# Performance work log

Measured on AMD Instinct MI355X. Metric: run time of the kernel, lower is better.

The kernel has to match this reference:

```python
import jax, jax.numpy as jnp
import numpy as np

BATCH = 8192
IN_DIM = 2048
OUT_DIM = 2048
DEPTH = 5


def setup_inputs() -> dict:
    key = jax.random.key(0)
    k1, k2, k3, k4 = jax.random.split(key, 4)
    x = jax.random.normal(k1, (BATCH, IN_DIM), dtype=jnp.float32)
    hyperdimensional_weights = jax.random.normal(k2, (DEPTH, IN_DIM, OUT_DIM), dtype=jnp.float32)
    classical_weights = jax.random.normal(k3, (IN_DIM, OUT_DIM), dtype=jnp.float32)
    classical_biases = jax.random.normal(k4, (OUT_DIM,), dtype=jnp.float32)
    return {
        "x": x,
        "hyperdimensional_weights": hyperdimensional_weights,
        "classical_weights": classical_weights,
        "classical_biases": classical_biases,
    }


def _hyperdimensional_probs(hd_w):
    # angle = W[d, j, 0], phase = W[d, j, 1] for output index j (j < input_dims)
    depth, in_dim, _ = hd_w.shape
    angles = hd_w[:, :OUT_DIM, 0]   # [depth, out]
    phases = hd_w[:, :OUT_DIM, 1]   # [depth, out]
    # Initial uniform state 1/sqrt(n), replicated per output unit j.
    s0 = jnp.full((OUT_DIM, in_dim), 1.0 / np.sqrt(in_dim), dtype=jnp.complex64)

    def step(s, ang_ph):
        ang, ph = ang_ph                      # each [out]
        c = jnp.cos(ang)[:, None]
        sn = jnp.sin(ang)[:, None]
        # Circulant rotation: new[k] = cos*s[k] - sin*s[k+1] + sin*s[k-1] (cyclic)
        s = c * s - sn * jnp.roll(s, -1, axis=1) + sn * jnp.roll(s, 1, axis=1)
        # Global phase gate: diag(e^{i*phase})
        s = s * jnp.exp(1j * ph)[:, None]
        return s, None

    s, _ = jax.lax.scan(step, s0, (angles, phases))
    # probability = |state[0]|^2
    return jnp.abs(s[:, 0]) ** 2              # [out], real float32


def reference(x, hyperdimensional_weights, classical_weights, classical_biases):
    classical = x @ classical_weights + classical_biases            # [B, out]
    hd = _hyperdimensional_probs(hyperdimensional_weights)          # [out] (batch-independent)
    return jnp.tanh(classical + hd[None, :])
```

## Files before the change

kernel.cpp:

```cpp
#include <hip/hip_runtime.h>

#define BATCH 8192
#define DIM   2048
#define DEPTH 5


#define BUFSZ  65536
#define ABYTES 32768

typedef short bf16x8_t __attribute__((ext_vector_type(8)));
typedef float f32x4_t  __attribute__((ext_vector_type(4)));

__device__ __forceinline__ unsigned short f2bf(float f) {
  unsigned u = __float_as_uint(f);
  u += 0x7fffu + ((u >> 16) & 1u);
  return (unsigned short)(u >> 16);
}
__device__ __forceinline__ float bf2f(unsigned short h) {
  return __uint_as_float(((unsigned)h) << 16);
}

__global__ void prep_fused_kernel(const float* __restrict__ x,
                                  const float* __restrict__ hdw,
                                  const float* __restrict__ W,
                                  const float* __restrict__ bias,
                                  float* __restrict__ bias2,
                                  unsigned short* __restrict__ xhi,
                                  unsigned short* __restrict__ xlo,
                                  unsigned short* __restrict__ whi,
                                  unsigned short* __restrict__ wlo) {
  __shared__ float tile[32][33];
  const int b = blockIdx.x;
  const int tid = threadIdx.x;

  if (b < 8192) {
    size_t g = (size_t)b * 256 + tid;
    const float4* xp = (const float4*)(x + g * 8);
    float4 v0 = xp[0], v1 = xp[1];
    float v[8] = {v0.x, v0.y, v0.z, v0.w, v1.x, v1.y, v1.z, v1.w};
    bf16x8_t h, lo;
#pragma unroll
    for (int j = 0; j < 8; ++j) {
      unsigned short hj = f2bf(v[j]);
      h[j] = (short)hj;
      lo[j] = (short)f2bf(v[j] - bf2f(hj));
    }
    ((bf16x8_t*)xhi)[g] = h;
    ((bf16x8_t*)xlo)[g] = lo;
  } else if (b < 12288) {
    const int t = b - 8192;
    const int k0 = (t >> 6) * 32;
    const int n0 = (t & 63) * 32;
    const int tx = tid & 31;
    const int ty = tid >> 5;
#pragma unroll
    for (int r = 0; r < 32; r += 8)
      tile[ty + r][tx] = W[(size_t)(k0 + ty + r) * DIM + n0 + tx];
    __syncthreads();
    const int n = tid >> 3;
    const int kq = (tid & 7) * 4;
    ushort4 hv, lv;
    float vv0 = tile[kq + 0][n], vv1 = tile[kq + 1][n];
    float vv2 = tile[kq + 2][n], vv3 = tile[kq + 3][n];
    hv.x = f2bf(vv0); lv.x = f2bf(vv0 - bf2f(hv.x));
    hv.y = f2bf(vv1); lv.y = f2bf(vv1 - bf2f(hv.y));
    hv.z = f2bf(vv2); lv.z = f2bf(vv2 - bf2f(hv.z));
    hv.w = f2bf(vv3); lv.w = f2bf(vv3 - bf2f(hv.w));
    const size_t o = (size_t)(n0 + n) * DIM + k0 + kq;
    *(ushort4*)(whi + o) = hv;
    *(ushort4*)(wlo + o) = lv;
  } else {
    int j = (b - 12288) * 256 + tid;
    float p = 1.0f;
#pragma unroll
    for (int d = 0; d < DEPTH; ++d)
      p *= cosf(hdw[(size_t)d * DIM * DIM + (size_t)j * DIM]);
    bias2[j] = bias[j] + p * p * (1.0f / 2048.0f);
  }
}

#define GLDS(SRC, OFF)                                                         \
  __builtin_amdgcn_global_load_lds(                                            \
      (const __attribute__((address_space(1))) unsigned int*)(SRC),            \
      (__attribute__((address_space(3))) unsigned int*)(smem + (OFF)), 16, 0, 0)

#define MFMA16(A, B, C) __builtin_amdgcn_mfma_f32_16x16x32_bf16((A), (B), (C), 0, 0, 0)

#define STAGE(KO, SO)                                                          \
  do {                                                                         \
    GLDS(sAh + (KO),             (SO) + 0              + wdst);                \
    GLDS(sAh + 128 * DIM + (KO), (SO) + 8192           + wdst);                \
    GLDS(sAl + (KO),             (SO) + 16384          + wdst);                \
    GLDS(sAl + 128 * DIM + (KO), (SO) + 24576          + wdst);                \
    GLDS(sBh + (KO),             (SO) + ABYTES + 0     + wdst);                \
    GLDS(sBh + 128 * DIM + (KO), (SO) + ABYTES + 8192  + wdst);                \
    GLDS(sBl + (KO),             (SO) + ABYTES + 16384 + wdst);                \
    GLDS(sBl + 128 * DIM + (KO), (SO) + ABYTES + 24576 + wdst);                \
  } while (0)

__global__ __launch_bounds__(512, 2) void gemm_pipe_kernel(
    const unsigned short* __restrict__ Ah, const unsigned short* __restrict__ Al,
    const unsigned short* __restrict__ Bh, const unsigned short* __restrict__ Bl,
    const float* __restrict__ bias2, float* __restrict__ out) {
  __shared__ float4 smem4[2 * BUFSZ / 16];
  char* smem = (char*)smem4;

  const int tid  = threadIdx.x;
  const int lane = tid & 63;
  const int wave = tid >> 6;
  const int wm   = wave >> 1;
  const int wn   = wave & 1;
  const int l15  = lane & 15;
  const int kl   = lane >> 4;
  const int bm = blockIdx.x;
  const int bn = blockIdx.y;

  const int rsub = wave * 16 + (lane >> 2);
  const int kg   = ((lane & 3) ^ ((lane >> 3) & 3)) * 8;
  const unsigned short* sAh = Ah + ((size_t)(bm * 256 + rsub)) * DIM + kg;
  const unsigned short* sAl = Al + ((size_t)(bm * 256 + rsub)) * DIM + kg;
  const unsigned short* sBh = Bh + ((size_t)(bn * 256 + rsub)) * DIM + kg;
  const unsigned short* sBl = Bl + ((size_t)(bn * 256 + rsub)) * DIM + kg;
  const unsigned wdst = wave * 1024;

  const int foff = l15 * 64 + ((kl * 16) ^ (((l15 >> 1) & 3) << 4));

  const f32x4_t vzero = {0.f, 0.f, 0.f, 0.f};
  f32x4_t acc[4][8];
#pragma unroll
  for (int i = 0; i < 4; ++i)
#pragma unroll
    for (int j = 0; j < 8; ++j) acc[i][j] = vzero;

  STAGE(0, 0);
  asm volatile("s_waitcnt vmcnt(0)" ::: "memory");
  asm volatile("s_barrier" ::: "memory");

#pragma unroll 1
  for (int t = 0; t < 64; ++t) {
    const unsigned bo = (unsigned)(t & 1) * BUFSZ;
    const unsigned so = bo ^ BUFSZ;

    if (t < 63) {
      const int ko = (t + 1) * 32;
      STAGE(ko, so);
    }

    const char* pA = smem + bo + wm * 4096 + foff;
    bf16x8_t ah[4], al[4];
#pragma unroll
    for (int mt = 0; mt < 4; ++mt) {
      ah[mt] = *(const bf16x8_t*)(pA + mt * 1024);
      al[mt] = *(const bf16x8_t*)(pA + 16384 + mt * 1024);
    }

    const char* pB = smem + bo + ABYTES + wn * 8192 + foff;

    {
      bf16x8_t bh[4], bl[4];
#pragma unroll
      for (int nt = 0; nt < 4; ++nt) {
        bh[nt] = *(const bf16x8_t*)(pB + nt * 1024);
        bl[nt] = *(const bf16x8_t*)(pB + 16384 + nt * 1024);
      }
      __builtin_amdgcn_s_setprio(1);
#pragma unroll
      for (int mt = 0; mt < 4; ++mt)
#pragma unroll
        for (int nt = 0; nt < 4; ++nt) {
          acc[mt][nt] = MFMA16(ah[mt], bh[nt], acc[mt][nt]);
          acc[mt][nt] = MFMA16(ah[mt], bl[nt], acc[mt][nt]);
          acc[mt][nt] = MFMA16(al[mt], bh[nt], acc[mt][nt]);
        }
      __builtin_amdgcn_s_setprio(0);
    }

    {
      bf16x8_t bh[4], bl[4];
#pragma unroll
      for (int nt = 0; nt < 4; ++nt) {
        bh[nt] = *(const bf16x8_t*)(pB + 4096 + nt * 1024);
        bl[nt] = *(const bf16x8_t*)(pB + 16384 + 4096 + nt * 1024);
      }
      __builtin_amdgcn_s_setprio(1);
#pragma unroll
      for (int mt = 0; mt < 4; ++mt)
#pragma unroll
        for (int nt = 0; nt < 4; ++nt) {
          acc[mt][4 + nt] = MFMA16(ah[mt], bh[nt], acc[mt][4 + nt]);
          acc[mt][4 + nt] = MFMA16(ah[mt], bl[nt], acc[mt][4 + nt]);
          acc[mt][4 + nt] = MFMA16(al[mt], bh[nt], acc[mt][4 + nt]);
        }
      __builtin_amdgcn_s_setprio(0);
    }

    if (t < 63) {
      asm volatile("s_waitcnt vmcnt(0)" ::: "memory");
      asm volatile("s_barrier" ::: "memory");
    }
  }

  const int orow0 = bm * 256 + wm * 64;
  const int ocol0 = bn * 256 + wn * 128;
#pragma unroll
  for (int nt = 0; nt < 8; ++nt) {
    const int col = ocol0 + nt * 16 + l15;
    const float b2 = bias2[col];
#pragma unroll
    for (int mt = 0; mt < 4; ++mt) {
      const int row = orow0 + mt * 16 + kl * 4;
#pragma unroll
      for (int r = 0; r < 4; ++r) {
        float z = acc[mt][nt][r] + b2;
        float e = __expf(2.0f * z);
        out[(size_t)(row + r) * DIM + col] = 1.0f - 2.0f / (e + 1.0f);
      }
    }
  }
}

extern "C" void kernel_launch(void* const* d_in, const int* in_sizes, int n_in,
                              void* d_out, int out_size, void* d_ws, size_t ws_size,
                              hipStream_t stream) {
  const float* x   = (const float*)d_in[0];
  const float* hdw = (const float*)d_in[1];
  const float* W   = (const float*)d_in[2];
  const float* b   = (const float*)d_in[3];
  float* out = (float*)d_out;

  char* ws = (char*)d_ws;
  unsigned short* xhi  = (unsigned short*)ws;
  unsigned short* xlo  = xhi + (size_t)BATCH * DIM;
  unsigned short* wThi = xlo + (size_t)BATCH * DIM;
  unsigned short* wTlo = wThi + (size_t)DIM * DIM;
  float*          bias2 = (float*)(wTlo + (size_t)DIM * DIM);

  prep_fused_kernel<<<12296, 256, 0, stream>>>(
      x, hdw, W, b, bias2, xhi, xlo, wThi, wTlo);
  gemm_pipe_kernel<<<dim3(BATCH / 256, DIM / 256), 512, 0, stream>>>(
      xhi, xlo, wThi, wTlo, bias2, out);
}
```

Measured before the change: 333.8 us.

## Software-pipeline LDS fragment reads across MFMA groups and iteration boundary

```diff
diff --git a/kernel.cpp b/kernel.cpp
--- a/kernel.cpp
+++ b/kernel.cpp
@@ -98,6 +98,29 @@
     GLDS(sBl + 128 * DIM + (KO), (SO) + ABYTES + 24576 + wdst);                \
   } while (0)
 
+#define READ_BQ(PB, NT, H0, L0, H1, L1)                                        \
+  do {                                                                         \
+    H0 = *(const bf16x8_t*)((PB) + (NT) * 1024);                               \
+    L0 = *(const bf16x8_t*)((PB) + 16384 + (NT) * 1024);                       \
+    H1 = *(const bf16x8_t*)((PB) + ((NT) + 1) * 1024);                         \
+    L1 = *(const bf16x8_t*)((PB) + 16384 + ((NT) + 1) * 1024);                 \
+  } while (0)
+
+#define QMFMA(H0, L0, H1, L1, C0)                                              \
+  do {                                                                         \
+    __builtin_amdgcn_s_setprio(1);                                             \
+    _Pragma("unroll")                                                          \
+    for (int mt = 0; mt < 4; ++mt) {                                           \
+      acc[mt][C0]     = MFMA16(A_h[mt], H0, acc[mt][C0]);                      \
+      acc[mt][C0]     = MFMA16(A_h[mt], L0, acc[mt][C0]);                      \
+      acc[mt][C0]     = MFMA16(A_l[mt], H0, acc[mt][C0]);                      \
+      acc[mt][C0 + 1] = MFMA16(A_h[mt], H1, acc[mt][C0 + 1]);                  \
+      acc[mt][C0 + 1] = MFMA16(A_h[mt], L1, acc[mt][C0 + 1]);                  \
+      acc[mt][C0 + 1] = MFMA16(A_l[mt], H1, acc[mt][C0 + 1]);                  \
+    }                                                                          \
+    __builtin_amdgcn_s_setprio(0);                                             \
+  } while (0)
+
 __global__ __launch_bounds__(512, 2) void gemm_pipe_kernel(
     const unsigned short* __restrict__ Ah, const unsigned short* __restrict__ Al,
     const unsigned short* __restrict__ Bh, const unsigned short* __restrict__ Bl,
@@ -132,71 +155,62 @@
 #pragma unroll
     for (int j = 0; j < 8; ++j) acc[i][j] = vzero;
 
+  bf16x8_t A_h[4], A_l[4];
+  bf16x8_t Bc_h0, Bc_l0, Bc_h1, Bc_l1;
+  bf16x8_t Bn_h0, Bn_l0, Bn_h1, Bn_l1;
+
   STAGE(0, 0);
   asm volatile("s_waitcnt vmcnt(0)" ::: "memory");
   asm volatile("s_barrier" ::: "memory");
+  {
+    const char* pA0 = smem + wm * 4096 + foff;
+#pragma unroll
+    for (int mt = 0; mt < 4; ++mt) {
+      A_h[mt] = *(const bf16x8_t*)(pA0 + mt * 1024);
+      A_l[mt] = *(const bf16x8_t*)(pA0 + 16384 + mt * 1024);
+    }
+    const char* pB0 = smem + ABYTES + wn * 8192 + foff;
+    READ_BQ(pB0, 0, Bc_h0, Bc_l0, Bc_h1, Bc_l1);
+  }
 
 #pragma unroll 1
   for (int t = 0; t < 64; ++t) {
     const unsigned bo = (unsigned)(t & 1) * BUFSZ;
     const unsigned so = bo ^ BUFSZ;
+    const char* pB = smem + bo + ABYTES + wn * 8192 + foff;
 
     if (t < 63) {
       const int ko = (t + 1) * 32;
       STAGE(ko, so);
     }
 
-    const char* pA = smem + bo + wm * 4096 + foff;
-    bf16x8_t ah[4], al[4];
-#pragma unroll
-    for (int mt = 0; mt < 4; ++mt) {
-      ah[mt] = *(const bf16x8_t*)(pA + mt * 1024);
-      al[mt] = *(const bf16x8_t*)(pA + 16384 + mt * 1024);
-    }
-
-    const char* pB = smem + bo + ABYTES + wn * 8192 + foff;
-
-    {
-      bf16x8_t bh[4], bl[4];
-#pragma unroll
-      for (int nt = 0; nt < 4; ++nt) {
-        bh[nt] = *(const bf16x8_t*)(pB + nt * 1024);
-        bl[nt] = *(const bf16x8_t*)(pB + 16384 + nt * 1024);
+    READ_BQ(pB, 2, Bn_h0, Bn_l0, Bn_h1, Bn_l1);
+    QMFMA(Bc_h0, Bc_l0, Bc_h1, Bc_l1, 0);
+
+    READ_BQ(pB, 4, Bc_h0, Bc_l0, Bc_h1, Bc_l1);
+    QMFMA(Bn_h0, Bn_l0, Bn_h1, Bn_l1, 2);
+
+    READ_BQ(pB, 6, Bn_h0, Bn_l0, Bn_h1, Bn_l1);
+    QMFMA(Bc_h0, Bc_l0, Bc_h1, Bc_l1, 4);
+
+    asm volatile("s_waitcnt lgkmcnt(0)" ::: "memory");
+    if (t < 63) { asm volatile("s_waitcnt vmcnt(0)" ::: "memory"); }
+    asm volatile("s_barrier" ::: "memory");
+
+    if (t < 63) {
+      const char* pBn = smem + so + ABYTES + wn * 8192 + foff;
+      READ_BQ(pBn, 0, Bc_h0, Bc_l0, Bc_h1, Bc_l1);
+    }
+
+    QMFMA(Bn_h0, Bn_l0, Bn_h1, Bn_l1, 6);
+
+    if (t < 63) {
+      const char* pAn = smem + so + wm * 4096 + foff;
+#pragma unroll
+      for (int mt = 0; mt < 4; ++mt) {
+        A_h[mt] = *(const bf16x8_t*)(pAn + mt * 1024);
+        A_l[mt] = *(const bf16x8_t*)(pAn + 16384 + mt * 1024);
       }
-      __builtin_amdgcn_s_setprio(1);
-#pragma unroll
-      for (int mt = 0; mt < 4; ++mt)
-#pragma unroll
-        for (int nt = 0; nt < 4; ++nt) {
-          acc[mt][nt] = MFMA16(ah[mt], bh[nt], acc[mt][nt]);
-          acc[mt][nt] = MFMA16(ah[mt], bl[nt], acc[mt][nt]);
-          acc[mt][nt] = MFMA16(al[mt], bh[nt], acc[mt][nt]);
-        }
-      __builtin_amdgcn_s_setprio(0);
-    }
-
-    {
-      bf16x8_t bh[4], bl[4];
-#pragma unroll
-      for (int nt = 0; nt < 4; ++nt) {
-        bh[nt] = *(const bf16x8_t*)(pB + 4096 + nt * 1024);
-        bl[nt] = *(const bf16x8_t*)(pB + 16384 + 4096 + nt * 1024);
-      }
-      __builtin_amdgcn_s_setprio(1);
-#pragma unroll
-      for (int mt = 0; mt < 4; ++mt)
-#pragma unroll
-        for (int nt = 0; nt < 4; ++nt) {
-          acc[mt][4 + nt] = MFMA16(ah[mt], bh[nt], acc[mt][4 + nt]);
-          acc[mt][4 + nt] = MFMA16(ah[mt], bl[nt], acc[mt][4 + nt]);
-          acc[mt][4 + nt] = MFMA16(al[mt], bh[nt], acc[mt][4 + nt]);
-        }
-      __builtin_amdgcn_s_setprio(0);
-    }
-
-    if (t < 63) {
-      asm volatile("s_waitcnt vmcnt(0)" ::: "memory");
-      asm volatile("s_barrier" ::: "memory");
     }
   }
 
```

Result: no change. 327.6 us, median of 2 (-1.8%).
